# Kernel optimization log

Hardware: AMD Instinct MI355X
Metric: run time of the kernel (lower is better)

The kernel has to match this reference:

```python
import jax, jax.numpy as jnp
import numpy as np

NUM_TAGS = 27
NEG = -100.0


def _build_tables():
    start = np.full(NUM_TAGS, NEG, np.float32)
    end = np.full(NUM_TAGS, NEG, np.float32)
    trans = np.full((NUM_TAGS, NUM_TAGS), NEG, np.float32)
    for i in [0, 5, 10, 15, 20, 25, 26]:
        start[i] = 0.0
    for i in range(4):
        for b in [0, 5, 10, 15, 20]:
            trans[b + i, b + 1 + i] = 0.0
    for i in [4, 9, 14, 19, 24]:
        trans[i, i] = 0.0
    trans[4, 26] = 0.0
    trans[9, 25] = 0.0
    trans[14, 26] = 0.0
    trans[19, 25] = 0.0
    trans[24, 25:] = 0.0
    trans[25, 0] = 0.0
    trans[25, 10] = 0.0
    trans[25, 25:] = 0.0
    trans[26, 5] = 0.0
    trans[26, 15] = 0.0
    trans[26, 25:] = 0.0
    for i in [4, 9, 14, 19, 24, 25, 26]:
        end[i] = 0.0
    repeats = np.array([10, 10, 5, 1, 1], np.int32)  # sums to 27
    mapping = np.repeat(np.arange(7), [5, 5, 5, 5, 5, 1, 1]).astype(np.int32)
    return jnp.asarray(start), jnp.asarray(end), jnp.asarray(trans), repeats, jnp.asarray(mapping)


def setup_inputs() -> dict:
    key = jax.random.key(0)
    B, C, L = 256, 5, 4096
    emissions = jax.random.normal(key, (B, C, L), dtype=jnp.float32)
    mask = jnp.ones((B, L), dtype=bool)
    return {"emissions": emissions, "mask": mask}


def reference(emissions, mask):
    start_t, end_t, trans, repeats, mapping = _build_tables()
    m = mask.T.astype(bool)                      # (L, B)
    em = jnp.transpose(emissions, (2, 0, 1))     # (L, B, 5)
    em = jnp.repeat(em, repeats, axis=2)         # (L, B, 27)
    L, B, T = em.shape

    score0 = start_t + em[0]                     # (B, T)

    def step(score, xs):
        em_i, m_i = xs
        # (B, prev, cur)
        ns = trans[None, :, :] + score[:, :, None] + em_i[:, None, :]
        idx = jnp.argmax(ns, axis=1).astype(jnp.int32)
        best = jnp.max(ns, axis=1)
        new_score = jnp.where(m_i[:, None], best, score)
        return new_score, idx

    score, hist = jax.lax.scan(step, score0, (em[1:], m[1:]))  # hist: (L-1, B, T)
    history = jnp.concatenate([hist, jnp.zeros((1, B, T), hist.dtype)], axis=0)  # (L, B, T)

    score = score + end_t
    end_tag = jnp.argmax(score, axis=1).astype(jnp.int32)       # (B,)
    seq_ends = m.sum(axis=0).astype(jnp.int32) - 1               # (B,)
    history = history.at[seq_ends, jnp.arange(B), :].set(end_tag[:, None])

    batch_idx = jnp.arange(B)

    def back(bt, h_row):
        bt = h_row[batch_idx, bt]
        return bt, bt

    _, tags = jax.lax.scan(back, jnp.zeros(B, jnp.int32), history, reverse=True)  # (L, B)
    decoded = tags.T                                             # (B, L)
    return mapping[decoded]
```

## Files before the change

kernel.cpp:

```cpp
#include <hip/hip_runtime.h>


constexpr int LQ = 4096;

__device__ const float ENDV27[27] = {
  -100,-100,-100,-100,0, -100,-100,-100,-100,0, -100,-100,-100,-100,0,
  -100,-100,-100,-100,0, -100,-100,-100,-100,0, 0, 0};

__device__ __forceinline__ float bperm(int addr, float v) {
  return __int_as_float(__builtin_amdgcn_ds_bpermute(addr, __float_as_int(v)));
}
template <int CTRL>
__device__ __forceinline__ float qperm(float v) {
  return __int_as_float(
      __builtin_amdgcn_update_dpp(0, __float_as_int(v), CTRL, 0xF, 0xF, false));
}

template <bool QP>
__device__ __forceinline__ void fwd_body(const float* __restrict__ em,
                                         unsigned* __restrict__ Hd,
                                         int* __restrict__ endtag) {
  const float NEGF = -1e30f;
  const int lane = threadIdx.x;
  const int k = lane & 3;
  const int g = lane >> 2;
  const int b = blockIdx.x * 16 + g;

  const bool kLt2 = (k < 2);
  const bool k0m = (k == 0);
  const bool k2m = (k == 2);

  const int qb = (lane & ~3) << 2;
  const int a1 = (lane ^ 1) << 2;
  const int a2 = (lane ^ 3) << 2;
  const int a3 = qb + (3 << 2);
  const int a4 = qb + ((((k == 0) | (k == 3)) ? 1 : 0) << 2);
  const int a5 = qb + (2 << 2);

  const int chA = kLt2 ? 0 : 1;
  const int chB = k0m ? 3 : ((k == 1) ? 4 : 2);
  const float* epA = em + ((size_t)b * 5 + chA) * LQ;
  const float* epB = em + ((size_t)b * 5 + chB) * LQ;

  float4 ea0 = *(const float4*)(epA + 0);
  float4 ea1 = *(const float4*)(epA + 4);
  float4 eb0 = *(const float4*)(epB + 0);
  float4 eb1 = *(const float4*)(epB + 4);

  float A0 = 0.f    + ea0.x;
  float A1 = -100.f + ea0.x;
  float A2 = -100.f + ea0.x;
  float A3 = -100.f + ea0.x;
  float A4 = -100.f + ea0.x;
  float B0 = ((k == 3) ? -100.f : 0.f) + eb0.x;
  float B1 = -100.f + eb0.x;
  float B2 = -100.f + eb0.x;

  unsigned wE = 0u, wH = 0u, w4 = 0u;

#define MSGS() do {                                                       \
    if constexpr (QP) {                                                   \
      M1 = qperm<0xB1>(A4);                                \
      M2 = qperm<0x1B>(A4);                                \
      M3 = qperm<0xFF>(B2);                                \
      M4 = qperm<0x41>(B0);                                \
      M5 = qperm<0xAA>(B1);                                \
    } else {                                                              \
      M1 = bperm(a1, A4); M2 = bperm(a2, A4); M3 = bperm(a3, B2);         \
      M4 = bperm(a4, B0); M5 = bperm(a5, B1);                             \
    }                                                                     \
  } while (0)

#define STEP(EA_, EB_, SH_) do {                                          \
    float M1, M2, M3, M4, M5;                                             \
    MSGS();                                                               \
    const float eA = (EA_), eB = (EB_);                                   \
                                       \
    const float nA1 = A0 + eA, nA2 = A1 + eA, nA3 = A2 + eA;              \
                      \
    const float qe0 = A3 + eA, qe1 = A4 + eA;                             \
    const float nA4 = fmaxf(qe0, qe1);                                    \
    wE |= ((unsigned)((qe0 == nA4) ? 0 : 1)) << (SH_);                    \
                                        \
    const float nA0 = (kLt2 ? B0 : M4) + eA;                              \
     \
    const float qh0 = M1 + eB, qh1 = M2 + eB, qh2 = M3 + eB;              \
    const float qh3 = (k0m ? B0 : M4) + eB;                               \
    const float qh4 = (k0m ? M4 : B0) + eB;                               \
    const float hmx = fmaxf(fmaxf(fmaxf(qh0, qh1), qh2), fmaxf(qh3, qh4)); \
    { int cd = 4;                                                         \
      cd = (qh3 == hmx) ? 3 : cd; cd = (qh2 == hmx) ? 2 : cd;             \
      cd = (qh1 == hmx) ? 1 : cd; cd = (qh0 == hmx) ? 0 : cd;             \
      wH |= ((unsigned)cd) << (SH_); }                                    \
                         \
    const float nB1 = B0 + eB;                                            \
                                        \
    const float q240 = B1 + eB, q241 = B2 + eB;                           \
    const float nB2 = fmaxf(q240, q241);                                  \
    w4 |= ((unsigned)((q240 == nB2) ? 0 : 1)) << (SH_);                   \
                   \
    const float nB0 = kLt2 ? hmx : (k2m ? NEGF : (M5 + eB));              \
    A0 = nA0; A1 = nA1; A2 = nA2; A3 = nA3; A4 = nA4;                     \
    B0 = nB0; B1 = nB1; B2 = nB2;                                         \
  } while (0)

  {
    float4 n0 = *(const float4*)(epA + 8);
    float4 n1 = *(const float4*)(epA + 12);
    float4 m0 = *(const float4*)(epB + 8);
    float4 m1 = *(const float4*)(epB + 12);
    asm volatile("" ::: "memory");
    STEP(ea0.y, eb0.y, 3);
    STEP(ea0.z, eb0.z, 6);
    STEP(ea0.w, eb0.w, 9);
    STEP(ea1.x, eb1.x, 12);
    STEP(ea1.y, eb1.y, 15);
    STEP(ea1.z, eb1.z, 18);
    STEP(ea1.w, eb1.w, 21);
    {
      unsigned* hb = Hd + ((size_t)b << 12);
      hb[k] = wE;
      if (k != 2) hb[k0m ? 5 : ((k == 1) ? 6 : 4)] = kLt2 ? wH : w4;
    }
    ea0 = n0; ea1 = n1; eb0 = m0; eb1 = m1;
  }

  for (int c = 1; c < 512; ++c) {
    const int tn = (c < 511) ? ((c + 1) << 3) : (c << 3);
    float4 n0 = *(const float4*)(epA + tn);
    float4 n1 = *(const float4*)(epA + tn + 4);
    float4 m0 = *(const float4*)(epB + tn);
    float4 m1 = *(const float4*)(epB + tn + 4);
    asm volatile("" ::: "memory");
    wE = 0u; wH = 0u; w4 = 0u;
    STEP(ea0.x, eb0.x, 0);
    STEP(ea0.y, eb0.y, 3);
    STEP(ea0.z, eb0.z, 6);
    STEP(ea0.w, eb0.w, 9);
    STEP(ea1.x, eb1.x, 12);
    STEP(ea1.y, eb1.y, 15);
    STEP(ea1.z, eb1.z, 18);
    STEP(ea1.w, eb1.w, 21);
    {
      unsigned* hb = Hd + ((size_t)b << 12) + (c << 3);
      hb[k] = wE;
      if (k != 2) hb[k0m ? 5 : ((k == 1) ? 6 : 4)] = kLt2 ? wH : w4;
    }
    ea0 = n0; ea1 = n1; eb0 = m0; eb1 = m1;
  }
#undef STEP
#undef MSGS

  __shared__ float fs[16][28];
  fs[g][5 * k + 0] = A0;
  fs[g][5 * k + 1] = A1;
  fs[g][5 * k + 2] = A2;
  fs[g][5 * k + 3] = A3;
  fs[g][5 * k + 4] = A4;
  fs[g][k0m ? 25 : ((k == 1) ? 26 : (k2m ? 20 : 22))] = B0;
  if (k >= 2) fs[g][k2m ? 21 : 23] = B1;
  if (k == 3) fs[g][24] = B2;
  __syncthreads();
  if (k == 0) {
    float bb = fs[g][0] + ENDV27[0];
    int bi = 0;
#pragma unroll
    for (int j = 1; j < 27; ++j) {
      float v = fs[g][j] + ENDV27[j];
      if (v > bb) { bb = v; bi = j; }
    }
    endtag[b] = bi;
  }
}

__global__ __launch_bounds__(64, 1) void viterbi_fwd(const float* __restrict__ em,
                                                     unsigned* __restrict__ Hd,
                                                     int* __restrict__ endtag) {
  const int lane = threadIdx.x;
  const int pq = __builtin_amdgcn_update_dpp(0, lane, 0xB1, 0xF, 0xF, false);
  const bool qp = (__all(pq == (lane ^ 1)) != 0);
  if (qp) fwd_body<true>(em, Hd, endtag);
  else    fwd_body<false>(em, Hd, endtag);
}

constexpr int SEG = 128;
constexpr int NSEG = LQ / SEG;

__device__ __forceinline__ int prevf(unsigned w, int s) {
  if (s == 25) { int c = (w >> 5) & 7;  return (c < 2) ? (9 + 10 * c) : (22 + c); }
  if (s == 26) { int c = (w >> 8) & 7;  return (c < 2) ? (4 + 10 * c) : (22 + c); }
  if (s < 25 && (s % 5) == 4) { int bit = (w >> (s / 5)) & 1; return bit ? s : s - 1; }
  if (s == 0 || s == 10) return 25;
  if (s == 5 || s == 15) return 26;
  return s - 1;
}

__device__ __forceinline__ int mapst(int s) { return (s < 25) ? (s / 5) : (s - 20); }

__device__ __forceinline__ int shof(int s) {
  return (s == 25) ? 5 : (s == 26) ? 8 : (s < 25 && (s % 5) == 4) ? (s / 5) : 0;
}

__global__ __launch_bounds__(896) void viterbi_back(const unsigned* __restrict__ Hd,
                                                    const int* __restrict__ endtag,
                                                    int* __restrict__ out) {
  const int b = blockIdx.x;
  __shared__ __align__(16) unsigned W[LQ];
  __shared__ __align__(16) int tags[LQ];
  __shared__ signed char exS[NSEG][27];
  __shared__ int entryS[NSEG];
  __shared__ unsigned LUTW[27 * 8];
  __shared__ unsigned SH0[27];

  const unsigned* Hb = Hd + ((size_t)b << 12);
  const int tid = threadIdx.x;

  if (tid < 27 * 8) {
    const int s = tid >> 3, c = tid & 7;
    unsigned wsyn;
    if (s == 25)      wsyn = (unsigned)c << 5;
    else if (s == 26) wsyn = (unsigned)c << 8;
    else if (s < 25 && (s % 5) == 4) wsyn = (unsigned)(c & 1) << (s / 5);
    else              wsyn = 0u;
    const int p = prevf(wsyn, s);
    LUTW[tid] = (unsigned)(p & 31) | ((unsigned)shof(p & 31) << 8) |
                ((unsigned)(mapst(p & 31) & 15) << 16);
  }
  if (tid < 27) SH0[tid] = (unsigned)shof(tid);

  for (int c = tid; c < 512; c += 896) {
    const uint4 q0 = *(const uint4*)(Hb + (c << 3));
    const uint4 q1 = *(const uint4*)(Hb + (c << 3) + 4);
    const unsigned d0 = q0.x, d1 = q0.y, d2 = q0.z, d3 = q0.w,
                   d4 = q1.x, d5 = q1.y, d6 = q1.z;
#pragma unroll
    for (int j = 0; j < 8; ++j) {
      const int sh = 3 * j;
      unsigned w = ((d0 >> sh) & 1u) | (((d1 >> sh) & 1u) << 1) |
                   (((d2 >> sh) & 1u) << 2) | (((d3 >> sh) & 1u) << 3) |
                   (((d4 >> sh) & 1u) << 4) | (((d5 >> sh) & 7u) << 5) |
                   (((d6 >> sh) & 7u) << 8);
      W[(c << 3) + j] = w;
    }
  }
  __syncthreads();

  const int seg = tid / 27;
  const int e = tid - seg * 27;

  if (tid < NSEG * 27) {
    const int lo = seg * SEG;
    const int hi = (seg == NSEG - 1) ? (LQ - 1) : (lo + SEG);
    int s = e;
    unsigned sh = SH0[s];
    for (int t = hi; t > lo; --t) {
      const unsigned w = W[t];
      const unsigned v = LUTW[(s << 3) + ((w >> sh) & 7u)];
      s = (int)(v & 31u); sh = (v >> 8) & 15u;
    }
    exS[seg][e] = (signed char)s;
  }
  __syncthreads();

  if (tid == 0) {
    int s = endtag[b];
    for (int kk = NSEG - 1; kk >= 0; --kk) { entryS[kk] = s; s = exS[kk][s]; }
  }
  __syncthreads();

  if (tid < NSEG * 27 && e == entryS[seg]) {
    const int lo = seg * SEG;
    const int hi = (seg == NSEG - 1) ? (LQ - 1) : (lo + SEG);
    int s = e;
    unsigned sh = SH0[s];
    if (seg == NSEG - 1) tags[LQ - 1] = mapst(s);
    for (int t = hi; t > lo; --t) {
      const unsigned w = W[t];
      const unsigned v = LUTW[(s << 3) + ((w >> sh) & 7u)];
      s = (int)(v & 31u); sh = (v >> 8) & 15u;
      tags[t - 1] = (int)((v >> 16) & 15u);
    }
  }
  __syncthreads();

  int4* outb = (int4*)(out + (size_t)b * LQ);
  const int4* tg = (const int4*)tags;
  for (int i = tid; i < LQ / 4; i += 896) outb[i] = tg[i];
}

extern "C" void kernel_launch(void* const* d_in, const int* in_sizes, int n_in,
                              void* d_out, int out_size, void* d_ws, size_t ws_size,
                              hipStream_t stream) {
  const float* em = (const float*)d_in[0];
  unsigned* Hd = (unsigned*)d_ws;
  int* endtag = (int*)((char*)d_ws + (5u << 20));
  int* out = (int*)d_out;

  viterbi_fwd<<<dim3(16), dim3(64), 0, stream>>>(em, Hd, endtag);
  viterbi_back<<<dim3(256), dim3(896), 0, stream>>>(Hd, endtag, out);
}
```

Before: 517.1 us.

## Shorten backtrace segments and resolve segment entries with parallel pointer-jumping

The backward kernel now uses 32-step segments, giving 128 segments. Each thread walks four segment/state pairs at once, interleaved to hide LDS latency. The serial single-thread chain over segment exit maps is replaced by a log-depth pointer-doubling composition in shared memory, which costs seven barriers. The forward loop also switches to incremented pointers and peels its last iteration to drop per-iteration index arithmetic.

```diff
diff --git a/kernel.cpp b/kernel.cpp
--- a/kernel.cpp
+++ b/kernel.cpp
@@ -29,6 +29,7 @@
   const bool kLt2 = (k < 2);
   const bool k0m = (k == 0);
   const bool k2m = (k == 2);
+  const int slotw = k0m ? 5 : ((k == 1) ? 6 : 4);
 
   const int qb = (lane & ~3) << 2;
   const int a1 = (lane ^ 1) << 2;
@@ -104,6 +105,17 @@
     B0 = nB0; B1 = nB1; B2 = nB2;                                         \
   } while (0)
 
+#define STEP8() do {                                                      \
+    STEP(ea0.x, eb0.x, 0);                                                \
+    STEP(ea0.y, eb0.y, 3);                                                \
+    STEP(ea0.z, eb0.z, 6);                                                \
+    STEP(ea0.w, eb0.w, 9);                                                \
+    STEP(ea1.x, eb1.x, 12);                                               \
+    STEP(ea1.y, eb1.y, 15);                                               \
+    STEP(ea1.z, eb1.z, 18);                                               \
+    STEP(ea1.w, eb1.w, 21);                                               \
+  } while (0)
+
   {
     float4 n0 = *(const float4*)(epA + 8);
     float4 n1 = *(const float4*)(epA + 12);
@@ -120,34 +132,32 @@
     {
       unsigned* hb = Hd + ((size_t)b << 12);
       hb[k] = wE;
-      if (k != 2) hb[k0m ? 5 : ((k == 1) ? 6 : 4)] = kLt2 ? wH : w4;
+      if (k != 2) hb[slotw] = kLt2 ? wH : w4;
     }
     ea0 = n0; ea1 = n1; eb0 = m0; eb1 = m1;
   }
 
-  for (int c = 1; c < 512; ++c) {
-    const int tn = (c < 511) ? ((c + 1) << 3) : (c << 3);
-    float4 n0 = *(const float4*)(epA + tn);
-    float4 n1 = *(const float4*)(epA + tn + 4);
-    float4 m0 = *(const float4*)(epB + tn);
-    float4 m1 = *(const float4*)(epB + tn + 4);
+  const float* pa = epA + 16;
+  const float* pb = epB + 16;
+  unsigned* hbp = Hd + ((size_t)b << 12) + 8;
+  for (int c = 1; c <= 510; ++c) {
+    float4 n0 = *(const float4*)(pa);
+    float4 n1 = *(const float4*)(pa + 4);
+    float4 m0 = *(const float4*)(pb);
+    float4 m1 = *(const float4*)(pb + 4);
     asm volatile("" ::: "memory");
     wE = 0u; wH = 0u; w4 = 0u;
-    STEP(ea0.x, eb0.x, 0);
-    STEP(ea0.y, eb0.y, 3);
-    STEP(ea0.z, eb0.z, 6);
-    STEP(ea0.w, eb0.w, 9);
-    STEP(ea1.x, eb1.x, 12);
-    STEP(ea1.y, eb1.y, 15);
-    STEP(ea1.z, eb1.z, 18);
-    STEP(ea1.w, eb1.w, 21);
-    {
-      unsigned* hb = Hd + ((size_t)b << 12) + (c << 3);
-      hb[k] = wE;
-      if (k != 2) hb[k0m ? 5 : ((k == 1) ? 6 : 4)] = kLt2 ? wH : w4;
-    }
+    STEP8();
+    hbp[k] = wE;
+    if (k != 2) hbp[slotw] = kLt2 ? wH : w4;
     ea0 = n0; ea1 = n1; eb0 = m0; eb1 = m1;
-  }
+    pa += 8; pb += 8; hbp += 8;
+  }
+  wE = 0u; wH = 0u; w4 = 0u;
+  STEP8();
+  hbp[k] = wE;
+  if (k != 2) hbp[slotw] = kLt2 ? wH : w4;
+#undef STEP8
 #undef STEP
 #undef MSGS
 
@@ -183,7 +193,7 @@
   else    fwd_body<false>(em, Hd, endtag);
 }
 
-constexpr int SEG = 128;
+constexpr int SEG = 32;
 constexpr int NSEG = LQ / SEG;
 
 __device__ __forceinline__ int prevf(unsigned w, int s) {
@@ -207,8 +217,7 @@
   const int b = blockIdx.x;
   __shared__ __align__(16) unsigned W[LQ];
   __shared__ __align__(16) int tags[LQ];
-  __shared__ signed char exS[NSEG][27];
-  __shared__ int entryS[NSEG];
+  __shared__ unsigned char EX[2][NSEG][27];
   __shared__ unsigned LUTW[27 * 8];
   __shared__ unsigned SH0[27];
 
@@ -245,35 +254,62 @@
   }
   __syncthreads();
 
-  const int seg = tid / 27;
-  const int e = tid - seg * 27;
-
-  if (tid < NSEG * 27) {
-    const int lo = seg * SEG;
-    const int hi = (seg == NSEG - 1) ? (LQ - 1) : (lo + SEG);
-    int s = e;
+  if (tid < 864) {
+    int sg0 = (tid) / 27,          e0 = (tid) - sg0 * 27;
+    int sg1 = (tid + 864) / 27,    e1 = (tid + 864) - sg1 * 27;
+    int sg2 = (tid + 1728) / 27,   e2 = (tid + 1728) - sg2 * 27;
+    int sg3 = (tid + 2592) / 27,   e3 = (tid + 2592) - sg3 * 27;
+    const int lo0 = sg0 * SEG, hi0 = (sg0 == NSEG - 1) ? (LQ - 1) : (lo0 + SEG);
+    const int lo1 = sg1 * SEG, hi1 = (sg1 == NSEG - 1) ? (LQ - 1) : (lo1 + SEG);
+    const int lo2 = sg2 * SEG, hi2 = (sg2 == NSEG - 1) ? (LQ - 1) : (lo2 + SEG);
+    const int lo3 = sg3 * SEG, hi3 = (sg3 == NSEG - 1) ? (LQ - 1) : (lo3 + SEG);
+    int s0 = e0, s1 = e1, s2 = e2, s3 = e3;
+    unsigned a0 = SH0[s0], a1 = SH0[s1], a2 = SH0[s2], a3 = SH0[s3];
+    for (int i = 0; i < SEG; ++i) {
+      const int t0 = hi0 - i, t1 = hi1 - i, t2 = hi2 - i, t3 = hi3 - i;
+      if (t0 > lo0) { const unsigned w = W[t0];
+        const unsigned v = LUTW[(s0 << 3) + ((w >> a0) & 7u)];
+        s0 = (int)(v & 31u); a0 = (v >> 8) & 15u; }
+      if (t1 > lo1) { const unsigned w = W[t1];
+        const unsigned v = LUTW[(s1 << 3) + ((w >> a1) & 7u)];
+        s1 = (int)(v & 31u); a1 = (v >> 8) & 15u; }
+      if (t2 > lo2) { const unsigned w = W[t2];
+        const unsigned v = LUTW[(s2 << 3) + ((w >> a2) & 7u)];
+        s2 = (int)(v & 31u); a2 = (v >> 8) & 15u; }
+      if (t3 > lo3) { const unsigned w = W[t3];
+        const unsigned v = LUTW[(s3 << 3) + ((w >> a3) & 7u)];
+        s3 = (int)(v & 31u); a3 = (v >> 8) & 15u; }
+    }
+    EX[0][sg0][e0] = (unsigned char)s0;
+    EX[0][sg1][e1] = (unsigned char)s1;
+    EX[0][sg2][e2] = (unsigned char)s2;
+    EX[0][sg3][e3] = (unsigned char)s3;
+  }
+
+  int cur = 0;
+  for (int d = 0; d < 7; ++d) {
+    const int stride = 1 << d;
+    __syncthreads();
+    for (int idx = tid; idx < NSEG * 27; idx += 896) {
+      const int kk = idx / 27, e = idx - kk * 27;
+      unsigned char v;
+      if (kk + stride < NSEG) v = EX[cur][kk][EX[cur][kk + stride][e]];
+      else                    v = EX[cur][kk][e];
+      EX[cur ^ 1][kk][e] = v;
+    }
+    cur ^= 1;
+  }
+  __syncthreads();
+
+  if (tid < NSEG) {
+    const int kk = tid;
+    const int endt = endtag[b];
+    const int ep = (kk == NSEG - 1) ? endt : (int)EX[cur][kk + 1][endt];
+    const int lo = kk * SEG;
+    const int hi = (kk == NSEG - 1) ? (LQ - 1) : (lo + SEG);
+    int s = ep;
     unsigned sh = SH0[s];
-    for (int t = hi; t > lo; --t) {
-      const unsigned w = W[t];
-      const unsigned v = LUTW[(s << 3) + ((w >> sh) & 7u)];
-      s = (int)(v & 31u); sh = (v >> 8) & 15u;
-    }
-    exS[seg][e] = (signed char)s;
-  }
-  __syncthreads();
-
-  if (tid == 0) {
-    int s = endtag[b];
-    for (int kk = NSEG - 1; kk >= 0; --kk) { entryS[kk] = s; s = exS[kk][s]; }
-  }
-  __syncthreads();
-
-  if (tid < NSEG * 27 && e == entryS[seg]) {
-    const int lo = seg * SEG;
-    const int hi = (seg == NSEG - 1) ? (LQ - 1) : (lo + SEG);
-    int s = e;
-    unsigned sh = SH0[s];
-    if (seg == NSEG - 1) tags[LQ - 1] = mapst(s);
+    if (kk == NSEG - 1) tags[LQ - 1] = mapst(s);
     for (int t = hi; t > lo; --t) {
       const unsigned w = W[t];
       const unsigned v = LUTW[(s << 3) + ((w >> sh) & 7u)];
```

Result: no change. 509.1 us (-1.5%).
